# Kernel optimization log

Hardware: AMD Instinct MI355X
Metric: run time of the kernel (lower is better)

Reference implementation:

```python
import jax, jax.numpy as jnp
import numpy as np
import math

T_LEN, BATCH, DIN, DH, DT = 512, 64, 512, 512, 128


def _u(key, shape, std):
    return jax.random.uniform(key, shape, jnp.float32, -std, std)


def setup_inputs() -> dict:
    key = jax.random.key(0)
    ks = jax.random.split(key, 32)
    std = 1.0 / math.sqrt(DH)
    inp = {
        'x': jax.random.normal(ks[0], (T_LEN, BATCH, DIN), jnp.float32),
        'topic': jax.random.normal(ks[1], (BATCH, DT), jnp.float32),
        'mask': jnp.ones((T_LEN, BATCH), jnp.float32),
        # weights stored as [in, out] (transpose of nn.Linear), uniform(-std, std)
        'W_x2zr': _u(ks[2], (DIN, 2 * DH), std),
        'W_tp2zr_x': _u(ks[3], (DT, 2 * DH), std),
        'W_xtp2z': _u(ks[4], (DH, DH), std),
        'b_xtp2z': _u(ks[5], (DH,), std),
        'W_xtp2r': _u(ks[6], (DH, DH), std),
        'b_xtp2r': _u(ks[7], (DH,), std),
        'W_h2zr': _u(ks[8], (DH, 2 * DH), std),
        'W_tp2zr_h': _u(ks[9], (DT, 2 * DH), std),
        'W_htp2z': _u(ks[10], (DH, DH), std),
        'W_htp2r': _u(ks[11], (DH, DH), std),
        'W_x2h': _u(ks[12], (DIN, DH), std),
        'W_tp2h_x': _u(ks[13], (DT, DH), std),
        'W_xtp2h': _u(ks[14], (DH, DH), std),
        'b_xtp2h': _u(ks[15], (DH,), std),
        'W_h2h': _u(ks[16], (DH, DH), std),
        'W_tp2h_h': _u(ks[17], (DT, DH), std),
        'W_htp2h': _u(ks[18], (DH, DH), std),
    }
    return inp


def _tpgru_forward(x, topic, mask,
                   W_x2zr, W_tp2zr_x, W_xtp2z, b_xtp2z, W_xtp2r, b_xtp2r,
                   W_h2zr, W_tp2zr_h, W_htp2z, W_htp2r,
                   W_x2h, W_tp2h_x, W_xtp2h, b_xtp2h,
                   W_h2h, W_tp2h_h, W_htp2h):
    # Precompute all time-parallel (input-side) projections outside the scan.
    ZR_x = x @ W_x2zr                          # [T,B,2H]
    tp_zr_x = topic @ W_tp2zr_x                # [B,2H]
    tp_zr_h = topic @ W_tp2zr_h                # [B,2H]
    Z_xtp, R_xtp = jnp.split(ZR_x * tp_zr_x[None], 2, axis=-1)
    ZR_xtp = jnp.concatenate([Z_xtp @ W_xtp2z + b_xtp2z,
                              R_xtp @ W_xtp2r + b_xtp2r], axis=-1)  # [T,B,2H]
    tp_h_x = topic @ W_tp2h_x                  # [B,H]
    tp_h_h = topic @ W_tp2h_h                  # [B,H]
    H_xtp = ((x @ W_x2h) * tp_h_x[None]) @ W_xtp2h + b_xtp2h        # [T,B,H]

    def step(h_, inputs):
        zr_xtp, h_xtp, m = inputs              # [B,2H], [B,H], [B]
        zr_htp = (h_ @ W_h2zr) * tp_zr_h
        z_htp, r_htp = jnp.split(zr_htp, 2, axis=-1)
        pre_zr = jax.nn.sigmoid(zr_xtp + jnp.concatenate(
            [z_htp @ W_htp2z, r_htp @ W_htp2r], axis=-1))
        z, r = jnp.split(pre_zr, 2, axis=-1)
        h = jnp.tanh(h_xtp + r * (((h_ @ W_h2h) * tp_h_h) @ W_htp2h))
        h = (1.0 - z) * h + z * h_
        m = m[:, None]
        h = m * h + (1.0 - m) * h_
        return h, h

    h0 = jnp.zeros((x.shape[1], W_h2h.shape[0]), x.dtype)
    hT, output = jax.lax.scan(step, h0, (ZR_xtp, H_xtp, mask))
    return output, hT[None]                    # [T,B,H], [1,B,H]


def reference(x, topic, mask,
              W_x2zr, W_tp2zr_x, W_xtp2z, b_xtp2z, W_xtp2r, b_xtp2r,
              W_h2zr, W_tp2zr_h, W_htp2z, W_htp2r,
              W_x2h, W_tp2h_x, W_xtp2h, b_xtp2h,
              W_h2h, W_tp2h_h, W_htp2h):
    return _tpgru_forward(x, topic, mask,
                          W_x2zr, W_tp2zr_x, W_xtp2z, b_xtp2z, W_xtp2r, b_xtp2r,
                          W_h2zr, W_tp2zr_h, W_htp2z, W_htp2r,
                          W_x2h, W_tp2h_x, W_xtp2h, b_xtp2h,
                          W_h2h, W_tp2h_h, W_htp2h)
```

## Files before the change

kernel.cpp:

```cpp
#include <hip/hip_runtime.h>
#include <stdint.h>
#include <stddef.h>


#define T_LEN 512
#define BATCH 64
#define DIN   512
#define DH    512
#define DT    128

typedef __attribute__((ext_vector_type(8))) short short8;
typedef __attribute__((ext_vector_type(4))) float f32x4;

static __device__ __forceinline__ float bf2f(unsigned short u) {
  unsigned v = ((unsigned)u) << 16;
  return __builtin_bit_cast(float, v);
}
static __device__ __forceinline__ unsigned short f2bf(float f) {
  unsigned v = __builtin_bit_cast(unsigned, f);
  unsigned r = (v + 0x7fffu + ((v >> 16) & 1u)) >> 16;
  return (unsigned short)r;
}
static __device__ __forceinline__ float sigmoid_f(float x) {
  return 1.f / (1.f + __expf(-x));
}
static __device__ __forceinline__ float tanh_f(float x) {
  float e = __expf(-2.f * fabsf(x));
  float t = (1.f - e) / (1.f + e);
  return copysignf(t, x);
}

template<bool F32>
static __device__ __forceinline__ void load8(const void* p, size_t off, unsigned short* d) {
  if (F32) {
    const float4* q = (const float4*)((const float*)p + off);
    float4 a = q[0], b = q[1];
    d[0] = f2bf(a.x); d[1] = f2bf(a.y); d[2] = f2bf(a.z); d[3] = f2bf(a.w);
    d[4] = f2bf(b.x); d[5] = f2bf(b.y); d[6] = f2bf(b.z); d[7] = f2bf(b.w);
  } else {
    *(uint4*)d = *(const uint4*)((const unsigned short*)p + off);
  }
}

__global__ __launch_bounds__(256) void k_topic(
    const float* __restrict__ topic,
    const float* __restrict__ Wzx,
    const float* __restrict__ Wzh,
    const float* __restrict__ Whx,
    const float* __restrict__ Whh,
    float* __restrict__ tzx, float* __restrict__ tzh,
    float* __restrict__ thx, float* __restrict__ thh)
{
  const int b = blockIdx.x;
  __shared__ float tp[DT];
  if (threadIdx.x < DT) tp[threadIdx.x] = topic[b * DT + threadIdx.x];
  __syncthreads();
  for (int c = threadIdx.x; c < 3072; c += 256) {
    const float* wp; float* op; int ld, cc;
    if (c < 1024)      { wp = Wzx; ld = 1024; cc = c;        op = &tzx[b*1024 + cc]; }
    else if (c < 2048) { wp = Wzh; ld = 1024; cc = c - 1024; op = &tzh[b*1024 + cc]; }
    else if (c < 2560) { wp = Whx; ld = 512;  cc = c - 2048; op = &thx[b*512  + cc]; }
    else               { wp = Whh; ld = 512;  cc = c - 2560; op = &thh[b*512  + cc]; }
    float acc = 0.f;
    #pragma unroll 4
    for (int k = 0; k < DT; ++k) acc += tp[k] * wp[(size_t)k * ld + cc];
    *op = acc;
  }
}

template<int EPI, bool AF32, bool BF32>
__global__ __launch_bounds__(256) void gemm64(
    const void* __restrict__ A, int lda,
    const void* __restrict__ B1, int ldb1,
    const float* __restrict__ rs1, int ldrs1,
    const float* __restrict__ bias,
    unsigned short* __restrict__ C, int ldc, int K)
{
  __shared__ unsigned short As[64][48];
  __shared__ unsigned short Bs[64][48];
  const int tid = threadIdx.x;
  const int n0 = blockIdx.x * 64;
  const int m0 = blockIdx.y * 64;
  const int wv = tid >> 6, lane = tid & 63;
  const int lh = lane & 15, q8 = (lane >> 4) * 8;
  const int arow = tid >> 2, acol = (tid & 3) * 8;
  const int brow = tid >> 3, bcol = (tid & 7) * 8;
  f32x4 acc[4] = {{0,0,0,0},{0,0,0,0},{0,0,0,0},{0,0,0,0}};

  for (int k0 = 0; k0 < K; k0 += 32) {
    unsigned short av[8], bv[8];
    load8<AF32>(A, (size_t)(m0 + arow) * lda + (k0 + acol), av);
    load8<BF32>(B1, (size_t)(k0 + brow) * ldb1 + (n0 + bcol), bv);
    __syncthreads();
    *(uint4*)(&As[arow][acol]) = *(const uint4*)av;
    #pragma unroll
    for (int i = 0; i < 8; ++i) Bs[bcol + i][brow] = bv[i];
    __syncthreads();
    short8 af = *(const short8*)(&As[wv * 16 + lh][q8]);
    #pragma unroll
    for (int nt = 0; nt < 4; ++nt) {
      short8 bf = *(const short8*)(&Bs[nt * 16 + lh][q8]);
      acc[nt] = __builtin_amdgcn_mfma_f32_16x16x32_bf16(af, bf, acc[nt], 0, 0, 0);
    }
  }

  #pragma unroll
  for (int nt = 0; nt < 4; ++nt) {
    #pragma unroll
    for (int r = 0; r < 4; ++r) {
      int row = m0 + wv * 16 + (lane >> 4) * 4 + r;
      int colc = nt * 16 + lh;
      float v = acc[nt][r];
      if (EPI == 0) v *= rs1[(size_t)(row & 63) * ldrs1 + (n0 + colc)];
      else          v += bias[n0 + colc];
      C[(size_t)row * ldc + (n0 + colc)] = f2bf(v);
    }
  }
}

__global__ __launch_bounds__(256) void k_comb(
    const float* __restrict__ W1, int ld1, int off1,
    const float* __restrict__ W2,
    const float* __restrict__ S, int ldS, int offS,
    unsigned short* __restrict__ Cout)
{
  __shared__ unsigned short As[64][48];
  __shared__ unsigned short Bs[64][48];
  const int tid = threadIdx.x;
  const int n0 = blockIdx.x * 64;
  const int m0 = blockIdx.y * 64;
  const int b  = blockIdx.z;
  const int wv = tid >> 6, lane = tid & 63;
  const int lh = lane & 15, q8 = (lane >> 4) * 8;
  const int arow = tid >> 2, acol = (tid & 3) * 8;
  const int brow = tid >> 3, bcol = (tid & 7) * 8;
  const float* sv = S + (size_t)b * ldS + offS;
  f32x4 acc[4] = {{0,0,0,0},{0,0,0,0},{0,0,0,0},{0,0,0,0}};

  for (int k0 = 0; k0 < 512; k0 += 32) {
    unsigned short av[8], bv[8];
    {
      const float* p = W1 + (size_t)(m0 + arow) * ld1 + off1 + k0 + acol;
      float4 a = ((const float4*)p)[0], c2 = ((const float4*)p)[1];
      av[0]=f2bf(a.x); av[1]=f2bf(a.y); av[2]=f2bf(a.z); av[3]=f2bf(a.w);
      av[4]=f2bf(c2.x); av[5]=f2bf(c2.y); av[6]=f2bf(c2.z); av[7]=f2bf(c2.w);
    }
    {
      float sk = sv[k0 + brow];
      const float* p = W2 + (size_t)(k0 + brow) * 512 + n0 + bcol;
      float4 a = ((const float4*)p)[0], c2 = ((const float4*)p)[1];
      bv[0]=f2bf(a.x*sk); bv[1]=f2bf(a.y*sk); bv[2]=f2bf(a.z*sk); bv[3]=f2bf(a.w*sk);
      bv[4]=f2bf(c2.x*sk); bv[5]=f2bf(c2.y*sk); bv[6]=f2bf(c2.z*sk); bv[7]=f2bf(c2.w*sk);
    }
    __syncthreads();
    *(uint4*)(&As[arow][acol]) = *(const uint4*)av;
    #pragma unroll
    for (int i = 0; i < 8; ++i) Bs[bcol + i][brow] = bv[i];
    __syncthreads();
    short8 af = *(const short8*)(&As[wv * 16 + lh][q8]);
    #pragma unroll
    for (int nt = 0; nt < 4; ++nt) {
      short8 bf = *(const short8*)(&Bs[nt * 16 + lh][q8]);
      acc[nt] = __builtin_amdgcn_mfma_f32_16x16x32_bf16(af, bf, acc[nt], 0, 0, 0);
    }
  }

  #pragma unroll
  for (int nt = 0; nt < 4; ++nt) {
    #pragma unroll
    for (int r = 0; r < 4; ++r) {
      int row = m0 + wv * 16 + (lane >> 4) * 4 + r;
      int col = n0 + nt * 16 + lh;
      Cout[(size_t)b * 262144 + (size_t)row * 512 + col] = f2bf(acc[nt][r]);
    }
  }
}

static __device__ __forceinline__ void accum8(float* a, float hk, uint4 v) {
  unsigned u0 = v.x, u1 = v.y, u2 = v.z, u3 = v.w;
  a[0] += hk * __builtin_bit_cast(float, u0 << 16);
  a[1] += hk * __builtin_bit_cast(float, u0 & 0xffff0000u);
  a[2] += hk * __builtin_bit_cast(float, u1 << 16);
  a[3] += hk * __builtin_bit_cast(float, u1 & 0xffff0000u);
  a[4] += hk * __builtin_bit_cast(float, u2 << 16);
  a[5] += hk * __builtin_bit_cast(float, u2 & 0xffff0000u);
  a[6] += hk * __builtin_bit_cast(float, u3 << 16);
  a[7] += hk * __builtin_bit_cast(float, u3 & 0xffff0000u);
}

__global__ __launch_bounds__(512) void k_scan3(
    const unsigned short* __restrict__ Az,
    const unsigned short* __restrict__ Ar,
    const unsigned short* __restrict__ Ah,
    const unsigned short* __restrict__ ZRx,
    const unsigned short* __restrict__ Hx,
    const float* __restrict__ mask,
    unsigned* __restrict__ pub,
    float* out)
{
  const int g = blockIdx.x;
  const int b = g >> 3;
  const int w = g & 7;
  const int c0 = w * 64;
  const int t = threadIdx.x;
  const int chunk = t & 7;
  const int ph = t >> 3;
  __shared__ float hs[512];
  __shared__ float part[64][8][25];
  __shared__ float red[192];

  const size_t mbase = (size_t)b * 262144 + (size_t)ph * 512 + c0 + chunk * 8;
  const unsigned short* pz0 = Az + mbase;
  const unsigned short* pr0 = Ar + mbase;
  const unsigned short* pv0 = Ah + mbase;

  unsigned* pubB0 = pub + (size_t)b * 512;
  unsigned* pubB1 = pub + (size_t)(64 + b) * 512;

  float hold = 0.f;
  for (int tm = 0; tm < T_LEN; ++tm) {
    unsigned* pubC = (tm & 1) ? pubB1 : pubB0;
    unsigned* pubP = (tm & 1) ? pubB0 : pubB1;
    const size_t itb = (size_t)tm * BATCH + b;

    float g_zx = 0.f, g_rx = 0.f, g_hx = 0.f, g_m = 0.f;
    if (t < 64) {
      int gc = c0 + t;
      g_zx = bf2f(ZRx[itb * 1024 + gc]);
      g_rx = bf2f(ZRx[itb * 1024 + 512 + gc]);
      g_hx = bf2f(Hx[itb * 512 + gc]);
      g_m  = mask[itb];
    }
    if (t < 8) {
      const unsigned* tagp = pubC + t * 64 + 32;
      while ((int)__hip_atomic_load(tagp, __ATOMIC_RELAXED, __HIP_MEMORY_SCOPE_AGENT) < tm)
        ;
    }
    __syncthreads();
    if (t < 256) {
      unsigned v = __hip_atomic_load(pubC + (t >> 5) * 64 + (t & 31),
                                     __ATOMIC_RELAXED, __HIP_MEMORY_SCOPE_AGENT);
      int col = (t >> 5) * 64 + (t & 31) * 2;
      hs[col]     = bf2f((unsigned short)(v & 0xffffu));
      hs[col + 1] = bf2f((unsigned short)(v >> 16));
    }
    __syncthreads();

    float az[8] = {0,0,0,0,0,0,0,0};
    float ar[8] = {0,0,0,0,0,0,0,0};
    float av[8] = {0,0,0,0,0,0,0,0};
    #pragma unroll
    for (int j = 0; j < 8; ++j) {
      float hk = hs[ph + 64 * j];
      uint4 vz = *(const uint4*)(pz0 + (size_t)j * 64 * 512);
      uint4 vr = *(const uint4*)(pr0 + (size_t)j * 64 * 512);
      uint4 vv = *(const uint4*)(pv0 + (size_t)j * 64 * 512);
      accum8(az, hk, vz);
      accum8(ar, hk, vr);
      accum8(av, hk, vv);
    }
    #pragma unroll
    for (int e = 0; e < 8; ++e) {
      part[ph][chunk][e]      = az[e];
      part[ph][chunk][8 + e]  = ar[e];
      part[ph][chunk][16 + e] = av[e];
    }
    __syncthreads();

    if (t < 192) {
      int c = t & 63;
      int ch = c >> 3;
      int e  = (t >> 6) * 8 + (c & 7);
      float s = 0.f;
      #pragma unroll 16
      for (int p = 0; p < 64; ++p) s += part[p][ch][e];
      red[t] = s;
    }
    __syncthreads();

    if (t < 64) {
      float z  = sigmoid_f(red[t] + g_zx);
      float r  = sigmoid_f(red[64 + t] + g_rx);
      float hv = tanh_f(g_hx + r * red[128 + t]);
      float hnew = (1.f - z) * hv + z * hold;
      hnew = g_m * hnew + (1.f - g_m) * hold;
      hold = hnew;
      int gc = c0 + t;
      out[itb * 512 + gc] = hnew;
      if (tm == T_LEN - 1)
        out[(size_t)T_LEN * BATCH * 512 + (size_t)b * 512 + gc] = hnew;
      int hb = (int)f2bf(hnew);
      unsigned lo = (unsigned)__shfl(hb, 2 * t);
      unsigned hi = (unsigned)__shfl(hb, 2 * t + 1);
      if (t < 32)
        __hip_atomic_store(pubP + w * 64 + t, lo | (hi << 16),
                           __ATOMIC_RELAXED, __HIP_MEMORY_SCOPE_AGENT);
      asm volatile("s_waitcnt vmcnt(0)" ::: "memory");
      if (t == 0)
        __hip_atomic_store(pubP + w * 64 + 32, (unsigned)(tm + 1),
                           __ATOMIC_RELAXED, __HIP_MEMORY_SCOPE_AGENT);
    }
  }
}

extern "C" void kernel_launch(void* const* d_in, const int* in_sizes, int n_in,
                              void* d_out, int out_size, void* d_ws, size_t ws_size,
                              hipStream_t stream) {
  (void)in_sizes; (void)n_in; (void)out_size; (void)ws_size;
  const float* x        = (const float*)d_in[0];
  const float* topic    = (const float*)d_in[1];
  const float* mask     = (const float*)d_in[2];
  const float* W_x2zr   = (const float*)d_in[3];
  const float* W_tp2zrx = (const float*)d_in[4];
  const float* W_xtp2z  = (const float*)d_in[5];
  const float* b_xtp2z  = (const float*)d_in[6];
  const float* W_xtp2r  = (const float*)d_in[7];
  const float* b_xtp2r  = (const float*)d_in[8];
  const float* W_h2zr   = (const float*)d_in[9];
  const float* W_tp2zrh = (const float*)d_in[10];
  const float* W_htp2z  = (const float*)d_in[11];
  const float* W_htp2r  = (const float*)d_in[12];
  const float* W_x2h    = (const float*)d_in[13];
  const float* W_tp2hx  = (const float*)d_in[14];
  const float* W_xtp2h  = (const float*)d_in[15];
  const float* b_xtp2h  = (const float*)d_in[16];
  const float* W_h2h    = (const float*)d_in[17];
  const float* W_tp2hh  = (const float*)d_in[18];
  const float* W_htp2h  = (const float*)d_in[19];
  float* out = (float*)d_out;

  char* w = (char*)d_ws;
  unsigned* pub = (unsigned*)w;      w += (size_t)2 * 64 * 8 * 64 * 4;
  float* tzx = (float*)w;           w += (size_t)BATCH * 1024 * 4;
  float* tzh = (float*)w;           w += (size_t)BATCH * 1024 * 4;
  float* thx = (float*)w;           w += (size_t)BATCH * 512 * 4;
  float* thh = (float*)w;           w += (size_t)BATCH * 512 * 4;
  unsigned short* ZRxtp = (unsigned short*)w; w += (size_t)T_LEN * BATCH * 1024 * 2;
  unsigned short* Hxtp  = (unsigned short*)w; w += (size_t)T_LEN * BATCH * 512 * 2;
  unsigned short* SCR   = (unsigned short*)w; w += (size_t)T_LEN * BATCH * 1024 * 2;
  unsigned short* AhM   = (unsigned short*)w; w += (size_t)BATCH * 512 * 512 * 2;
  unsigned short* ZRs = SCR;
  unsigned short* Xhs = SCR;
  unsigned short* AzM = SCR;
  unsigned short* ArM = SCR + (size_t)BATCH * 512 * 512;

  const int M = T_LEN * BATCH;

  hipMemsetAsync(pub, 0, (size_t)2 * 64 * 8 * 64 * 4, stream);

  k_topic<<<BATCH, 256, 0, stream>>>(topic, W_tp2zrx, W_tp2zrh, W_tp2hx, W_tp2hh,
                                     tzx, tzh, thx, thh);
  gemm64<0, true, true><<<dim3(1024/64, M/64), 256, 0, stream>>>(
      x, DIN, W_x2zr, 1024, tzx, 1024, nullptr, ZRs, 1024, DIN);
  gemm64<1, false, true><<<dim3(512/64, M/64), 256, 0, stream>>>(
      ZRs, 1024, W_xtp2z, 512, nullptr, 0, b_xtp2z, ZRxtp, 1024, 512);
  gemm64<1, false, true><<<dim3(512/64, M/64), 256, 0, stream>>>(
      ZRs + 512, 1024, W_xtp2r, 512, nullptr, 0, b_xtp2r, ZRxtp + 512, 1024, 512);
  gemm64<0, true, true><<<dim3(512/64, M/64), 256, 0, stream>>>(
      x, DIN, W_x2h, 512, thx, 512, nullptr, Xhs, 512, DIN);
  gemm64<1, false, true><<<dim3(512/64, M/64), 256, 0, stream>>>(
      Xhs, 512, W_xtp2h, 512, nullptr, 0, b_xtp2h, Hxtp, 512, 512);

  k_comb<<<dim3(8, 8, 64), 256, 0, stream>>>(W_h2zr, 1024,   0, W_htp2z, tzh, 1024,   0, AzM);
  k_comb<<<dim3(8, 8, 64), 256, 0, stream>>>(W_h2zr, 1024, 512, W_htp2r, tzh, 1024, 512, ArM);
  k_comb<<<dim3(8, 8, 64), 256, 0, stream>>>(W_h2h,   512,   0, W_htp2h, thh,  512,   0, AhM);

  k_scan3<<<512, 512, 0, stream>>>(AzM, ArM, AhM, ZRxtp, Hxtp, mask,
                                   pub, out);
}
```

Baseline: 4.185 ms.

## Keep recurrent weight slices resident in registers across scan steps with wider blocks

Recurrent scan blocks now each own 128 output columns (4 blocks per batch row instead of 8) and load their slice of the three combined recurrent matrices into registers once before the time loop. This removes the per-step reload of the batched recurrent weights from memory. The tag wait is spread over more threads to drop a barrier, and gate inputs and outputs are handled as packed pairs. Holding 48 uint4 values per thread creates high register pressure and a risk of scratch spills under the 2-blocks launch bound.

Result: slower. 16.04 ms (+283.2%).

```diff
diff --git a/kernel.cpp b/kernel.cpp
--- a/kernel.cpp
+++ b/kernel.cpp
@@ -188,7 +188,7 @@
   a[7] += hk * __builtin_bit_cast(float, u3 & 0xffff0000u);
 }
 
-__global__ __launch_bounds__(512) void k_scan3(
+__global__ __launch_bounds__(512, 2) void k_scan4(
     const unsigned short* __restrict__ Az,
     const unsigned short* __restrict__ Ar,
     const unsigned short* __restrict__ Ah,
@@ -199,50 +199,53 @@
     float* out)
 {
   const int g = blockIdx.x;
-  const int b = g >> 3;
-  const int w = g & 7;
-  const int c0 = w * 64;
+  const int b = g >> 2;
+  const int w = g & 3;
+  const int c0 = w * 128;
   const int t = threadIdx.x;
-  const int chunk = t & 7;
-  const int ph = t >> 3;
+  const int chunk = t & 15;
+  const int ph = t >> 4;
   __shared__ float hs[512];
-  __shared__ float part[64][8][25];
-  __shared__ float red[192];
-
-  const size_t mbase = (size_t)b * 262144 + (size_t)ph * 512 + c0 + chunk * 8;
-  const unsigned short* pz0 = Az + mbase;
-  const unsigned short* pr0 = Ar + mbase;
-  const unsigned short* pv0 = Ah + mbase;
-
-  unsigned* pubB0 = pub + (size_t)b * 512;
-  unsigned* pubB1 = pub + (size_t)(64 + b) * 512;
-
-  float hold = 0.f;
+  __shared__ float part[32][16][25];
+  __shared__ float red[384];
+
+  const size_t abase = (size_t)b * 262144 + (size_t)ph * 512 + c0 + chunk * 8;
+  uint4 za[16], ra[16], va[16];
+  #pragma unroll
+  for (int j = 0; j < 16; ++j) {
+    za[j] = *(const uint4*)(Az + abase + (size_t)j * 32 * 512);
+    ra[j] = *(const uint4*)(Ar + abase + (size_t)j * 32 * 512);
+    va[j] = *(const uint4*)(Ah + abase + (size_t)j * 32 * 512);
+  }
+
+  unsigned* pubB0 = pub + (size_t)b * 320;
+  unsigned* pubB1 = pub + (size_t)(64 + b) * 320;
+
+  float hold0 = 0.f, hold1 = 0.f;
+
   for (int tm = 0; tm < T_LEN; ++tm) {
     unsigned* pubC = (tm & 1) ? pubB1 : pubB0;
     unsigned* pubP = (tm & 1) ? pubB0 : pubB1;
     const size_t itb = (size_t)tm * BATCH + b;
 
-    float g_zx = 0.f, g_rx = 0.f, g_hx = 0.f, g_m = 0.f;
+    unsigned p_zx = 0, p_rx = 0, p_hx = 0; float g_m = 0.f;
     if (t < 64) {
-      int gc = c0 + t;
-      g_zx = bf2f(ZRx[itb * 1024 + gc]);
-      g_rx = bf2f(ZRx[itb * 1024 + 512 + gc]);
-      g_hx = bf2f(Hx[itb * 512 + gc]);
+      int gc = c0 + 2 * t;
+      p_zx = *(const unsigned*)(ZRx + itb * 1024 + gc);
+      p_rx = *(const unsigned*)(ZRx + itb * 1024 + 512 + gc);
+      p_hx = *(const unsigned*)(Hx + itb * 512 + gc);
       g_m  = mask[itb];
     }
-    if (t < 8) {
-      const unsigned* tagp = pubC + t * 64 + 32;
+    if (t < 256) {
+      const unsigned* tagp = pubC + (t >> 6) * 80 + 64;
       while ((int)__hip_atomic_load(tagp, __ATOMIC_RELAXED, __HIP_MEMORY_SCOPE_AGENT) < tm)
         ;
-    }
-    __syncthreads();
-    if (t < 256) {
-      unsigned v = __hip_atomic_load(pubC + (t >> 5) * 64 + (t & 31),
+      unsigned v = __hip_atomic_load(pubC + (t >> 6) * 80 + (t & 63),
                                      __ATOMIC_RELAXED, __HIP_MEMORY_SCOPE_AGENT);
-      int col = (t >> 5) * 64 + (t & 31) * 2;
-      hs[col]     = bf2f((unsigned short)(v & 0xffffu));
-      hs[col + 1] = bf2f((unsigned short)(v >> 16));
+      float2 hv;
+      hv.x = bf2f((unsigned short)(v & 0xffffu));
+      hv.y = bf2f((unsigned short)(v >> 16));
+      *(float2*)(&hs[2 * t]) = hv;
     }
     __syncthreads();
 
@@ -250,14 +253,11 @@
     float ar[8] = {0,0,0,0,0,0,0,0};
     float av[8] = {0,0,0,0,0,0,0,0};
     #pragma unroll
-    for (int j = 0; j < 8; ++j) {
-      float hk = hs[ph + 64 * j];
-      uint4 vz = *(const uint4*)(pz0 + (size_t)j * 64 * 512);
-      uint4 vr = *(const uint4*)(pr0 + (size_t)j * 64 * 512);
-      uint4 vv = *(const uint4*)(pv0 + (size_t)j * 64 * 512);
-      accum8(az, hk, vz);
-      accum8(ar, hk, vr);
-      accum8(av, hk, vv);
+    for (int j = 0; j < 16; ++j) {
+      float hk = hs[ph + 32 * j];
+      accum8(az, hk, za[j]);
+      accum8(ar, hk, ra[j]);
+      accum8(av, hk, va[j]);
     }
     #pragma unroll
     for (int e = 0; e < 8; ++e) {
@@ -267,38 +267,39 @@
     }
     __syncthreads();
 
-    if (t < 192) {
-      int c = t & 63;
-      int ch = c >> 3;
-      int e  = (t >> 6) * 8 + (c & 7);
+    if (t < 384) {
+      int m = t >> 7, c = t & 127;
       float s = 0.f;
-      #pragma unroll 16
-      for (int p = 0; p < 64; ++p) s += part[p][ch][e];
-      red[t] = s;
+      #pragma unroll
+      for (int p = 0; p < 32; ++p) s += part[p][c >> 3][m * 8 + (c & 7)];
+      red[(m << 7) + c] = s;
     }
     __syncthreads();
 
     if (t < 64) {
-      float z  = sigmoid_f(red[t] + g_zx);
-      float r  = sigmoid_f(red[64 + t] + g_rx);
-      float hv = tanh_f(g_hx + r * red[128 + t]);
-      float hnew = (1.f - z) * hv + z * hold;
-      hnew = g_m * hnew + (1.f - g_m) * hold;
-      hold = hnew;
-      int gc = c0 + t;
-      out[itb * 512 + gc] = hnew;
-      if (tm == T_LEN - 1)
-        out[(size_t)T_LEN * BATCH * 512 + (size_t)b * 512 + gc] = hnew;
-      int hb = (int)f2bf(hnew);
-      unsigned lo = (unsigned)__shfl(hb, 2 * t);
-      unsigned hi = (unsigned)__shfl(hb, 2 * t + 1);
-      if (t < 32)
-        __hip_atomic_store(pubP + w * 64 + t, lo | (hi << 16),
-                           __ATOMIC_RELAXED, __HIP_MEMORY_SCOPE_AGENT);
+      int c = 2 * t;
+      float z0 = sigmoid_f(red[c]       + bf2f((unsigned short)(p_zx & 0xffffu)));
+      float z1 = sigmoid_f(red[c + 1]   + bf2f((unsigned short)(p_zx >> 16)));
+      float r0 = sigmoid_f(red[128 + c] + bf2f((unsigned short)(p_rx & 0xffffu)));
+      float r1 = sigmoid_f(red[129 + c] + bf2f((unsigned short)(p_rx >> 16)));
+      float hv0 = tanh_f(bf2f((unsigned short)(p_hx & 0xffffu)) + r0 * red[256 + c]);
+      float hv1 = tanh_f(bf2f((unsigned short)(p_hx >> 16))     + r1 * red[257 + c]);
+      float hn0 = (1.f - z0) * hv0 + z0 * hold0;
+      float hn1 = (1.f - z1) * hv1 + z1 * hold1;
+      hn0 = g_m * hn0 + (1.f - g_m) * hold0;
+      hn1 = g_m * hn1 + (1.f - g_m) * hold1;
+      hold0 = hn0; hold1 = hn1;
+      unsigned pk = (unsigned)f2bf(hn0) | ((unsigned)f2bf(hn1) << 16);
+      __hip_atomic_store(pubP + w * 80 + t, pk,
+                         __ATOMIC_RELAXED, __HIP_MEMORY_SCOPE_AGENT);
       asm volatile("s_waitcnt vmcnt(0)" ::: "memory");
       if (t == 0)
-        __hip_atomic_store(pubP + w * 64 + 32, (unsigned)(tm + 1),
+        __hip_atomic_store(pubP + w * 80 + 64, (unsigned)(tm + 1),
                            __ATOMIC_RELAXED, __HIP_MEMORY_SCOPE_AGENT);
+      float2 o; o.x = hn0; o.y = hn1;
+      *(float2*)(out + itb * 512 + c0 + c) = o;
+      if (tm == T_LEN - 1)
+        *(float2*)(out + (size_t)T_LEN * BATCH * 512 + (size_t)b * 512 + c0 + c) = o;
     }
   }
 }
@@ -330,7 +331,7 @@
   float* out = (float*)d_out;
 
   char* w = (char*)d_ws;
-  unsigned* pub = (unsigned*)w;      w += (size_t)2 * 64 * 8 * 64 * 4;
+  unsigned* pub = (unsigned*)w;      w += (size_t)2 * 64 * 4 * 80 * 4;
   float* tzx = (float*)w;           w += (size_t)BATCH * 1024 * 4;
   float* tzh = (float*)w;           w += (size_t)BATCH * 1024 * 4;
   float* thx = (float*)w;           w += (size_t)BATCH * 512 * 4;
@@ -346,7 +347,7 @@
 
   const int M = T_LEN * BATCH;
 
-  hipMemsetAsync(pub, 0, (size_t)2 * 64 * 8 * 64 * 4, stream);
+  hipMemsetAsync(pub, 0, (size_t)2 * 64 * 4 * 80 * 4, stream);
 
   k_topic<<<BATCH, 256, 0, stream>>>(topic, W_tp2zrx, W_tp2zrh, W_tp2hx, W_tp2hh,
                                      tzx, tzh, thx, thh);
@@ -365,6 +366,6 @@
   k_comb<<<dim3(8, 8, 64), 256, 0, stream>>>(W_h2zr, 1024, 512, W_htp2r, tzh, 1024, 512, ArM);
   k_comb<<<dim3(8, 8, 64), 256, 0, stream>>>(W_h2h,   512,   0, W_htp2h, thh,  512,   0, AhM);
 
-  k_scan3<<<512, 512, 0, stream>>>(AzM, ArM, AhM, ZRxtp, Hxtp, mask,
+  k_scan4<<<256, 512, 0, stream>>>(AzM, ArM, AhM, ZRxtp, Hxtp, mask,
                                    pub, out);
 }
```

## Pre-convert x and weights to bf16 and use 128x128 tiled MFMA GEMMs

Applied to the files above, without the earlier changes.

Adds kernels that convert x to bf16 once and transpose the projection weights into bf16 [N,K] layout. The input-projection GEMMs move from 64x64 to 128x128 tiles, with each wave computing a 4x4 grid of MFMA tiles, so each shared-memory fragment is reused more often. Both operands now load with vectorized stores, which removes the per-element transposed LDS writes and the in-loop fp32-to-bf16 conversions. The cost is extra conversion and transpose launches plus extra workspace; the bf16 copy of x reuses the AhM buffer before k_comb writes it.

After: 4.180 ms. Within noise of the previous version (-0.1%).

```diff
diff --git a/kernel.cpp b/kernel.cpp
--- a/kernel.cpp
+++ b/kernel.cpp
@@ -30,16 +30,30 @@
   return copysignf(t, x);
 }
 
-template<bool F32>
-static __device__ __forceinline__ void load8(const void* p, size_t off, unsigned short* d) {
-  if (F32) {
-    const float4* q = (const float4*)((const float*)p + off);
-    float4 a = q[0], b = q[1];
+__global__ __launch_bounds__(256) void k_cvt(const float* __restrict__ src,
+                                             unsigned short* __restrict__ dst,
+                                             int n8) {
+  for (int idx = blockIdx.x * 256 + threadIdx.x; idx < n8; idx += gridDim.x * 256) {
+    const float4* s = (const float4*)src + 2 * (size_t)idx;
+    float4 a = s[0], b = s[1];
+    unsigned short d[8];
     d[0] = f2bf(a.x); d[1] = f2bf(a.y); d[2] = f2bf(a.z); d[3] = f2bf(a.w);
     d[4] = f2bf(b.x); d[5] = f2bf(b.y); d[6] = f2bf(b.z); d[7] = f2bf(b.w);
-  } else {
-    *(uint4*)d = *(const uint4*)((const unsigned short*)p + off);
-  }
+    *(uint4*)(dst + (size_t)idx * 8) = *(const uint4*)d;
+  }
+}
+
+__global__ __launch_bounds__(256) void k_tr(const float* __restrict__ src,
+                                            unsigned short* __restrict__ dst,
+                                            int K, int N) {
+  __shared__ float t[32][33];
+  const int tx = threadIdx.x & 31, ty = threadIdx.x >> 5;
+  const int k0 = blockIdx.y * 32, n0 = blockIdx.x * 32;
+  for (int i = ty; i < 32; i += 8)
+    t[i][tx] = src[(size_t)(k0 + i) * N + n0 + tx];
+  __syncthreads();
+  for (int i = ty; i < 32; i += 8)
+    dst[(size_t)(n0 + i) * K + k0 + tx] = f2bf(t[tx][i]);
 }
 
 __global__ __launch_bounds__(256) void k_topic(
@@ -68,54 +82,66 @@
   }
 }
 
-template<int EPI, bool AF32, bool BF32>
-__global__ __launch_bounds__(256) void gemm64(
-    const void* __restrict__ A, int lda,
-    const void* __restrict__ B1, int ldb1,
-    const float* __restrict__ rs1, int ldrs1,
+template<int EPI>
+__global__ __launch_bounds__(256) void gemm128(
+    const unsigned short* __restrict__ A, int lda,
+    const unsigned short* __restrict__ BT, int ldb,
+    const float* __restrict__ rs, int ldrs,
     const float* __restrict__ bias,
     unsigned short* __restrict__ C, int ldc, int K)
 {
-  __shared__ unsigned short As[64][48];
-  __shared__ unsigned short Bs[64][48];
+  __shared__ unsigned short As[128][48];
+  __shared__ unsigned short Bs[128][48];
   const int tid = threadIdx.x;
-  const int n0 = blockIdx.x * 64;
-  const int m0 = blockIdx.y * 64;
+  const int n0 = blockIdx.x * 128;
+  const int m0 = blockIdx.y * 128;
   const int wv = tid >> 6, lane = tid & 63;
-  const int lh = lane & 15, q8 = (lane >> 4) * 8;
-  const int arow = tid >> 2, acol = (tid & 3) * 8;
-  const int brow = tid >> 3, bcol = (tid & 7) * 8;
-  f32x4 acc[4] = {{0,0,0,0},{0,0,0,0},{0,0,0,0},{0,0,0,0}};
+  const int lh = lane & 15, quad = lane >> 4, q8 = quad * 8;
+  const int wr = wv >> 1, wc = wv & 1;
+  const int srow = tid >> 1, scol = (tid & 1) * 16;
+
+  f32x4 acc[4][4] = {};
 
   for (int k0 = 0; k0 < K; k0 += 32) {
-    unsigned short av[8], bv[8];
-    load8<AF32>(A, (size_t)(m0 + arow) * lda + (k0 + acol), av);
-    load8<BF32>(B1, (size_t)(k0 + brow) * ldb1 + (n0 + bcol), bv);
-    __syncthreads();
-    *(uint4*)(&As[arow][acol]) = *(const uint4*)av;
-    #pragma unroll
-    for (int i = 0; i < 8; ++i) Bs[bcol + i][brow] = bv[i];
-    __syncthreads();
-    short8 af = *(const short8*)(&As[wv * 16 + lh][q8]);
-    #pragma unroll
-    for (int nt = 0; nt < 4; ++nt) {
-      short8 bf = *(const short8*)(&Bs[nt * 16 + lh][q8]);
-      acc[nt] = __builtin_amdgcn_mfma_f32_16x16x32_bf16(af, bf, acc[nt], 0, 0, 0);
-    }
+    uint4 a4[2], b4[2];
+    {
+      const unsigned short* ap = A  + (size_t)(m0 + srow) * lda + k0 + scol;
+      const unsigned short* bp = BT + (size_t)(n0 + srow) * ldb + k0 + scol;
+      a4[0] = ((const uint4*)ap)[0]; a4[1] = ((const uint4*)ap)[1];
+      b4[0] = ((const uint4*)bp)[0]; b4[1] = ((const uint4*)bp)[1];
+    }
+    __syncthreads();
+    *(uint4*)(&As[srow][scol])     = a4[0];
+    *(uint4*)(&As[srow][scol + 8]) = a4[1];
+    *(uint4*)(&Bs[srow][scol])     = b4[0];
+    *(uint4*)(&Bs[srow][scol + 8]) = b4[1];
+    __syncthreads();
+    short8 af[4], bf[4];
+    #pragma unroll
+    for (int i = 0; i < 4; ++i) {
+      af[i] = *(const short8*)(&As[wr * 64 + i * 16 + lh][q8]);
+      bf[i] = *(const short8*)(&Bs[wc * 64 + i * 16 + lh][q8]);
+    }
+    #pragma unroll
+    for (int i = 0; i < 4; ++i)
+      #pragma unroll
+      for (int j = 0; j < 4; ++j)
+        acc[i][j] = __builtin_amdgcn_mfma_f32_16x16x32_bf16(af[i], bf[j], acc[i][j], 0, 0, 0);
   }
 
   #pragma unroll
-  for (int nt = 0; nt < 4; ++nt) {
-    #pragma unroll
-    for (int r = 0; r < 4; ++r) {
-      int row = m0 + wv * 16 + (lane >> 4) * 4 + r;
-      int colc = nt * 16 + lh;
-      float v = acc[nt][r];
-      if (EPI == 0) v *= rs1[(size_t)(row & 63) * ldrs1 + (n0 + colc)];
-      else          v += bias[n0 + colc];
-      C[(size_t)row * ldc + (n0 + colc)] = f2bf(v);
-    }
-  }
+  for (int i = 0; i < 4; ++i)
+    #pragma unroll
+    for (int j = 0; j < 4; ++j)
+      #pragma unroll
+      for (int r = 0; r < 4; ++r) {
+        int row = m0 + wr * 64 + i * 16 + quad * 4 + r;
+        int col = n0 + wc * 64 + j * 16 + lh;
+        float v = acc[i][j][r];
+        if (EPI == 0) v *= rs[(size_t)(row & 63) * ldrs + col];
+        else          v += bias[col];
+        C[(size_t)row * ldc + col] = f2bf(v);
+      }
 }
 
 __global__ __launch_bounds__(256) void k_comb(
@@ -339,27 +365,40 @@
   unsigned short* Hxtp  = (unsigned short*)w; w += (size_t)T_LEN * BATCH * 512 * 2;
   unsigned short* SCR   = (unsigned short*)w; w += (size_t)T_LEN * BATCH * 1024 * 2;
   unsigned short* AhM   = (unsigned short*)w; w += (size_t)BATCH * 512 * 512 * 2;
+  unsigned short* WzrT  = (unsigned short*)w; w += (size_t)1024 * 512 * 2;
+  unsigned short* WzT   = (unsigned short*)w; w += (size_t)512 * 512 * 2;
+  unsigned short* WrT   = (unsigned short*)w; w += (size_t)512 * 512 * 2;
+  unsigned short* WxhT  = (unsigned short*)w; w += (size_t)512 * 512 * 2;
+  unsigned short* WhpT  = (unsigned short*)w; w += (size_t)512 * 512 * 2;
   unsigned short* ZRs = SCR;
   unsigned short* Xhs = SCR;
   unsigned short* AzM = SCR;
   unsigned short* ArM = SCR + (size_t)BATCH * 512 * 512;
+  unsigned short* xb  = AhM;
 
   const int M = T_LEN * BATCH;
 
   hipMemsetAsync(pub, 0, (size_t)2 * 64 * 8 * 64 * 4, stream);
+
+  k_cvt<<<2048, 256, 0, stream>>>(x, xb, (int)((size_t)M * DIN / 8));
+  k_tr<<<dim3(1024/32, 512/32), 256, 0, stream>>>(W_x2zr,  WzrT, 512, 1024);
+  k_tr<<<dim3( 512/32, 512/32), 256, 0, stream>>>(W_xtp2z, WzT,  512,  512);
+  k_tr<<<dim3( 512/32, 512/32), 256, 0, stream>>>(W_xtp2r, WrT,  512,  512);
+  k_tr<<<dim3( 512/32, 512/32), 256, 0, stream>>>(W_x2h,   WxhT, 512,  512);
+  k_tr<<<dim3( 512/32, 512/32), 256, 0, stream>>>(W_xtp2h, WhpT, 512,  512);
 
   k_topic<<<BATCH, 256, 0, stream>>>(topic, W_tp2zrx, W_tp2zrh, W_tp2hx, W_tp2hh,
                                      tzx, tzh, thx, thh);
-  gemm64<0, true, true><<<dim3(1024/64, M/64), 256, 0, stream>>>(
-      x, DIN, W_x2zr, 1024, tzx, 1024, nullptr, ZRs, 1024, DIN);
-  gemm64<1, false, true><<<dim3(512/64, M/64), 256, 0, stream>>>(
-      ZRs, 1024, W_xtp2z, 512, nullptr, 0, b_xtp2z, ZRxtp, 1024, 512);
-  gemm64<1, false, true><<<dim3(512/64, M/64), 256, 0, stream>>>(
-      ZRs + 512, 1024, W_xtp2r, 512, nullptr, 0, b_xtp2r, ZRxtp + 512, 1024, 512);
-  gemm64<0, true, true><<<dim3(512/64, M/64), 256, 0, stream>>>(
-      x, DIN, W_x2h, 512, thx, 512, nullptr, Xhs, 512, DIN);
-  gemm64<1, false, true><<<dim3(512/64, M/64), 256, 0, stream>>>(
-      Xhs, 512, W_xtp2h, 512, nullptr, 0, b_xtp2h, Hxtp, 512, 512);
+  gemm128<0><<<dim3(1024/128, M/128), 256, 0, stream>>>(
+      xb, DIN, WzrT, 512, tzx, 1024, nullptr, ZRs, 1024, DIN);
+  gemm128<1><<<dim3(512/128, M/128), 256, 0, stream>>>(
+      ZRs, 1024, WzT, 512, nullptr, 0, b_xtp2z, ZRxtp, 1024, 512);
+  gemm128<1><<<dim3(512/128, M/128), 256, 0, stream>>>(
+      ZRs + 512, 1024, WrT, 512, nullptr, 0, b_xtp2r, ZRxtp + 512, 1024, 512);
+  gemm128<0><<<dim3(512/128, M/128), 256, 0, stream>>>(
+      xb, DIN, WxhT, 512, thx, 512, nullptr, Xhs, 512, DIN);
+  gemm128<1><<<dim3(512/128, M/128), 256, 0, stream>>>(
+      Xhs, 512, WhpT, 512, nullptr, 0, b_xtp2h, Hxtp, 512, 512);
 
   k_comb<<<dim3(8, 8, 64), 256, 0, stream>>>(W_h2zr, 1024,   0, W_htp2z, tzh, 1024,   0, AzM);
   k_comb<<<dim3(8, 8, 64), 256, 0, stream>>>(W_h2zr, 1024, 512, W_htp2r, tzh, 1024, 512, ArM);
```
